# Optimization experiments

Hardware: AMD Instinct MI355X
Metric: run time of the kernel (lower is better)

## Reference

```python
import jax, jax.numpy as jnp
import numpy as np

BITS = 32  # container = uint32 -> 32 bits per word


def _pack_sign_bits(x):
    """Faithful jax port of np.signbit -> np.packbits -> .view(uint32).

    np.packbits is MSB-first within each byte; .view(uint32) then
    reinterprets groups of 4 bytes little-endian. We reproduce both.
    """
    n = x.shape[0]
    pad = (-n) % BITS  # zero-pad to a multiple of 32 (numpy.resize fills 0)
    if pad:
        x = jnp.concatenate([x, jnp.zeros((pad,), dtype=x.dtype)])
    bits = jnp.signbit(x).astype(jnp.uint32).reshape(-1, 4, 8)  # [words, byte, bit]
    bit_w = jnp.left_shift(jnp.uint32(1), (7 - jnp.arange(8)).astype(jnp.uint32))   # MSB-first in byte
    byte_w = jnp.left_shift(jnp.uint32(1), (8 * jnp.arange(4)).astype(jnp.uint32))  # little-endian bytes
    weights = byte_w[:, None] * bit_w[None, :]  # [4, 8] uint32
    return jnp.sum(bits * weights[None, :, :], axis=(1, 2), dtype=jnp.uint32)  # [n/32] uint32


def setup_inputs() -> dict:
    key = jax.random.key(0)
    N = 134217728  # 2^27 floats, multiple of 32
    x = jax.random.normal(key, (N,), dtype=jnp.float32)
    return {"x": x}


def reference(x):
    return _pack_sign_bits(x)
```

## Files before the change

### kernel.cpp

```cpp
#include <hip/hip_runtime.h>
#include <stdint.h>


__global__ __launch_bounds__(256) void PackBits_61289183314094_kernel(
    const uint4* __restrict__ x4, uint32_t* __restrict__ out, int n4) {
  int gid = blockIdx.x * blockDim.x + threadIdx.x;
  if (gid >= n4) return;

  uint4 v = x4[gid];

  int lane = threadIdx.x & 63;
  uint32_t nib = (v.x >> 31) | ((v.y >> 31) << 1) | ((v.z >> 31) << 2) |
                 ((v.w >> 31) << 3);
  uint32_t part = nib << (4 * (lane & 7));
  part |= __shfl_xor(part, 1);
  part |= __shfl_xor(part, 2);
  part |= __shfl_xor(part, 4);

  if ((lane & 7) == 0) {
    out[gid >> 3] = __builtin_bswap32(__brev(part));
  }
}

extern "C" void kernel_launch(void* const* d_in, const int* in_sizes, int n_in,
                              void* d_out, int out_size, void* d_ws, size_t ws_size,
                              hipStream_t stream) {
  const uint4* x4 = (const uint4*)d_in[0];
  uint32_t* out = (uint32_t*)d_out;
  int n = in_sizes[0];
  int n4 = n / 4;

  const int threads = 256;
  int blocks = (n4 + threads - 1) / threads;
  PackBits_61289183314094_kernel<<<blocks, threads, 0, stream>>>(x4, out, n4);
}
```

Baseline: 656.1 us.

## Pack sign bits with wave ballots over many scalar loads per thread

Each thread now issues 32 coalesced scalar nontemporal loads instead of one uint4 load, and the wave builds sign masks with __ballot. Lanes then select and bit-reverse their 32-bit word, which replaces the shuffle-reduction. Each lane writes one output word with a coalesced nontemporal store. The goal is more bytes in flight per thread and full-lane stores in a bandwidth-bound kernel, in exchange for scalar rather than vector loads and more registers.

```diff
diff --git a/kernel.cpp b/kernel.cpp
--- a/kernel.cpp
+++ b/kernel.cpp
@@ -2,35 +2,81 @@
 #include <stdint.h>
 
 
-__global__ __launch_bounds__(256) void PackBits_61289183314094_kernel(
-    const uint4* __restrict__ x4, uint32_t* __restrict__ out, int n4) {
-  int gid = blockIdx.x * blockDim.x + threadIdx.x;
-  if (gid >= n4) return;
+typedef uint32_t u32;
+typedef unsigned long long u64;
 
-  uint4 v = x4[gid];
+#define THREADS 256
+#define ROUNDS  8
+#define WAVE_FLOATS  (ROUNDS * 256)
+#define BLOCK_FLOATS (4 * WAVE_FLOATS)
 
-  int lane = threadIdx.x & 63;
-  uint32_t nib = (v.x >> 31) | ((v.y >> 31) << 1) | ((v.z >> 31) << 2) |
-                 ((v.w >> 31) << 3);
-  uint32_t part = nib << (4 * (lane & 7));
-  part |= __shfl_xor(part, 1);
-  part |= __shfl_xor(part, 2);
-  part |= __shfl_xor(part, 4);
+__global__ __launch_bounds__(THREADS) void PackBits_61289183314094_kernel(
+    const int* __restrict__ x, u32* __restrict__ out, int n) {
+  const int wave = threadIdx.x >> 6;
+  const int lane = threadIdx.x & 63;
+  const int fbase = blockIdx.x * BLOCK_FLOATS + wave * WAVE_FLOATS;
 
-  if ((lane & 7) == 0) {
-    out[gid >> 3] = __builtin_bswap32(__brev(part));
+  if (fbase + WAVE_FLOATS <= n) {
+    const int* p = x + fbase + lane;
+    int v[ROUNDS][4];
+#pragma unroll
+    for (int j = 0; j < ROUNDS; ++j)
+#pragma unroll
+      for (int k = 0; k < 4; ++k)
+        v[j][k] = __builtin_nontemporal_load(&p[j * 256 + k * 64]);
+
+    u32 w = 0;
+#pragma unroll
+    for (int j = 0; j < ROUNDS; ++j) {
+      u64 m0 = __ballot(v[j][0] < 0);
+      u64 m1 = __ballot(v[j][1] < 0);
+      u64 m2 = __ballot(v[j][2] < 0);
+      u64 m3 = __ballot(v[j][3] < 0);
+      u64 ma = ((lane >> 1) & 1) ? m1 : m0;
+      u64 mb = ((lane >> 1) & 1) ? m3 : m2;
+      u64 m  = ((lane >> 2) & 1) ? mb : ma;
+      u32 nat = (lane & 1) ? (u32)(m >> 32) : (u32)m;
+      if ((lane >> 3) == j) w = __builtin_bswap32(__brev(nat));
+    }
+    __builtin_nontemporal_store(w, &out[(fbase >> 5) + lane]);
+  } else {
+    const int nwords = (n + 31) >> 5;
+    u32 w = 0;
+#pragma unroll
+    for (int j = 0; j < ROUNDS; ++j) {
+      u64 m0 = 0, m1 = 0, m2 = 0, m3 = 0;
+      {
+        int i0 = fbase + j * 256 + 0 * 64 + lane;
+        int i1 = fbase + j * 256 + 1 * 64 + lane;
+        int i2 = fbase + j * 256 + 2 * 64 + lane;
+        int i3 = fbase + j * 256 + 3 * 64 + lane;
+        int v0 = (i0 < n) ? x[i0] : 0;
+        int v1 = (i1 < n) ? x[i1] : 0;
+        int v2 = (i2 < n) ? x[i2] : 0;
+        int v3 = (i3 < n) ? x[i3] : 0;
+        m0 = __ballot(v0 < 0);
+        m1 = __ballot(v1 < 0);
+        m2 = __ballot(v2 < 0);
+        m3 = __ballot(v3 < 0);
+      }
+      u64 ma = ((lane >> 1) & 1) ? m1 : m0;
+      u64 mb = ((lane >> 1) & 1) ? m3 : m2;
+      u64 m  = ((lane >> 2) & 1) ? mb : ma;
+      u32 nat = (lane & 1) ? (u32)(m >> 32) : (u32)m;
+      if ((lane >> 3) == j) w = __builtin_bswap32(__brev(nat));
+    }
+    int wi = (fbase >> 5) + lane;
+    if (wi < nwords) out[wi] = w;
   }
 }
 
 extern "C" void kernel_launch(void* const* d_in, const int* in_sizes, int n_in,
                               void* d_out, int out_size, void* d_ws, size_t ws_size,
                               hipStream_t stream) {
-  const uint4* x4 = (const uint4*)d_in[0];
-  uint32_t* out = (uint32_t*)d_out;
+  const int* x = (const int*)d_in[0];
+  u32* out = (u32*)d_out;
   int n = in_sizes[0];
-  int n4 = n / 4;
 
-  const int threads = 256;
-  int blocks = (n4 + threads - 1) / threads;
-  PackBits_61289183314094_kernel<<<blocks, threads, 0, stream>>>(x4, out, n4);
+  int blocks = (n + BLOCK_FLOATS - 1) / BLOCK_FLOATS;
+  PackBits_61289183314094_kernel<<<blocks, THREADS, 0, stream>>>(x, out, n);
 }
```

Result: no change. 655.4 us (-0.1%).
